# Kernel tuning notes

Hardware: AMD Instinct MI355X
Metric: run time of the kernel (lower is better)

Reference implementation:

```python
import jax, jax.numpy as jnp
import numpy as np

N = 500_000  # n_nodes == n_edges (required by the broadcast out * norm[:, None])
C_IN = 128
C_OUT = 128


def setup_inputs() -> dict:
    key = jax.random.key(0)
    k_x, k_e, k_w, k_b = jax.random.split(key, 4)
    x = jax.random.normal(k_x, (N, C_IN), dtype=jnp.float32)
    edge_index = jax.random.randint(k_e, (2, N), 0, N, dtype=jnp.int64)
    # Linear(in_channels, out_channels): weight [out, in], bias [out]
    bound = 1.0 / np.sqrt(C_IN)
    W = jax.random.uniform(k_w, (C_OUT, C_IN), minval=-bound, maxval=bound, dtype=jnp.float32)
    b = jax.random.uniform(k_b, (C_OUT,), minval=-bound, maxval=bound, dtype=jnp.float32)
    return {"x": x, "edge_index": edge_index, "W": W, "b": b}


def reference(x, edge_index, W, b):
    row, col = edge_index[0], edge_index[1]  # each [E], with E == N
    n = x.shape[0]
    out = x @ W.T + b  # [N, C_OUT]
    # degree via scatter-add of ones over row
    deg = jax.ops.segment_sum(jnp.ones(row.shape[0], dtype=x.dtype), row, num_segments=n)
    deg_inv_sqrt = jnp.where(deg > 0, jax.lax.rsqrt(jnp.where(deg > 0, deg, 1.0)), 0.0)
    norm = deg_inv_sqrt[row] * deg_inv_sqrt[col]  # [E] == [N]
    out = out * norm[:, None]  # broadcast relies on E == N (as in the torch source)
    # aggregated[row] += out[col]
    aggregated = jnp.zeros_like(out).at[row].add(out[col])
    return aggregated
```

## Files before the change

kernel.cpp:

```cpp
#include <hip/hip_runtime.h>

#define C 128

typedef __bf16 bf16_t;
typedef bf16_t bf16x8 __attribute__((ext_vector_type(8)));
typedef float f32x4 __attribute__((ext_vector_type(4)));

__global__ void deg_kernel(const int* __restrict__ row, int* __restrict__ deg, int e) {
    int i = blockIdx.x * blockDim.x + threadIdx.x;
    if (i < e) atomicAdd(&deg[row[i]], 1);
}

__global__ void wcvt_kernel(const float* __restrict__ W, bf16_t* __restrict__ Wb) {
    int i = blockIdx.x * blockDim.x + threadIdx.x;
    if (i < C * C) Wb[i] = (bf16_t)W[i];
}

__global__ __launch_bounds__(256) void scan1_kernel(const int* __restrict__ deg,
                                                    float* __restrict__ dis,
                                                    int* __restrict__ offs,
                                                    int* __restrict__ partials,
                                                    int* __restrict__ dhist, int n) {
    __shared__ int s[256];
    __shared__ int dh[32];
    const int tid = threadIdx.x;
    if (tid < 32) dh[tid] = 0;
    const int base = blockIdx.x * 1024 + tid * 4;
    int v[4];
    #pragma unroll
    for (int j = 0; j < 4; ++j) v[j] = (base + j < n) ? deg[base + j] : 0;
    #pragma unroll
    for (int j = 0; j < 4; ++j)
        if (base + j < n) dis[base + j] = v[j] > 0 ? rsqrtf((float)v[j]) : 0.f;
    int tsum = v[0] + v[1] + v[2] + v[3];
    s[tid] = tsum;
    __syncthreads();
    #pragma unroll
    for (int j = 0; j < 4; ++j)
        if (base + j < n) atomicAdd(&dh[min(v[j], 31)], 1);
    for (int off = 1; off < 256; off <<= 1) {
        int t = (tid >= off) ? s[tid - off] : 0;
        __syncthreads();
        s[tid] += t;
        __syncthreads();
    }
    int excl = s[tid] - tsum;
    #pragma unroll
    for (int j = 0; j < 4; ++j) {
        if (base + j < n) offs[base + j] = excl;
        excl += v[j];
    }
    if (tid == 255) partials[blockIdx.x] = s[255];
    if (tid < 32 && dh[tid] > 0) atomicAdd(&dhist[tid], dh[tid]);
}

__global__ __launch_bounds__(1024) void scan2_kernel(int* __restrict__ partials,
                                                     const int* __restrict__ dhist,
                                                     int* __restrict__ drun, int nb) {
    __shared__ int s[1024];
    const int tid = threadIdx.x;
    int v = (tid < nb) ? partials[tid] : 0;
    s[tid] = v;
    __syncthreads();
    for (int off = 1; off < 1024; off <<= 1) {
        int t = (tid >= off) ? s[tid - off] : 0;
        __syncthreads();
        s[tid] += t;
        __syncthreads();
    }
    if (tid < nb) partials[tid] = s[tid] - v;
    if (tid < 64) {
        int h = (tid < 32) ? dhist[tid] : 0;
        int c = h;
        #pragma unroll
        for (int off = 1; off < 32; off <<= 1) {
            int t = __shfl_up(c, off);
            if (tid >= off) c += t;
        }
        if (tid < 32) drun[tid] = c - h;
    }
}

__global__ __launch_bounds__(256) void permute_kernel(const int* __restrict__ deg,
                                                      int* __restrict__ drun,
                                                      int* __restrict__ perm, int n) {
    __shared__ int lh[32], lb[32];
    const int tid = threadIdx.x;
    const int i = blockIdx.x * 256 + tid;
    if (tid < 32) lh[tid] = 0;
    __syncthreads();
    int bin = 0, lr = 0;
    const bool valid = i < n;
    if (valid) {
        int d = deg[i];
        bin = min(d, 31);
        lr = atomicAdd(&lh[bin], 1);
    }
    __syncthreads();
    if (tid < 32 && lh[tid] > 0) lb[tid] = atomicAdd(&drun[tid], lh[tid]);
    __syncthreads();
    if (valid) perm[lb[bin] + lr] = i;
}

__global__ void bucket_kernel(const int* __restrict__ row, const int* __restrict__ col,
                              const int* __restrict__ offs, const int* __restrict__ partials,
                              const float* __restrict__ dis, int* __restrict__ cursor,
                              int2* __restrict__ csr_cw, int e) {
    int i = blockIdx.x * blockDim.x + threadIdx.x;
    if (i < e) {
        int r = row[i];
        int c = col[i];
        float w = dis[row[c]] * dis[col[c]];
        int pos = atomicAdd(&cursor[r], 1);
        int idx = offs[r] + partials[r >> 10] + pos;
        csr_cw[idx] = make_int2(c, __float_as_int(w));
    }
}

__global__ __launch_bounds__(256, 4) void fused_kernel(
        const f32x4* __restrict__ x4, const int2* __restrict__ csr_cw,
        const int* __restrict__ offs, const int* __restrict__ partials,
        const int* __restrict__ deg, const int* __restrict__ perm,
        const bf16x8* __restrict__ Wb8, const float* __restrict__ bias,
        float* __restrict__ out, int n)
{
    const int lane = threadIdx.x & 63;
    const int wave = threadIdx.x >> 6;
    const int m    = lane & 15;
    const int quad = lane >> 4;
    const long r0  = ((long)blockIdx.x * 4 + wave) * 16;
    if (r0 >= n) return;
    const int  pi = (int)r0 + m;
    const bool rv = pi < n;
    const int  prow  = rv ? perm[pi] : 0;
    const int  d     = rv ? deg[prow] : 0;
    const int  start = rv ? offs[prow] + partials[prow >> 10] : 0;

    f32x4 acc[8];
    #pragma unroll
    for (int i = 0; i < 8; ++i) acc[i] = (f32x4){0.f, 0.f, 0.f, 0.f};
    float sw = 0.f;

    int k = 0;
    for (; k + 2 <= d; k += 2) {
        const int2 cw0 = csr_cw[start + k];
        const int2 cw1 = csr_cw[start + k + 1];
        const float w0 = __int_as_float(cw0.y);
        const float w1 = __int_as_float(cw1.y);
        sw += w0 + w1;
        const f32x4* xr0 = x4 + (long)cw0.x * 32 + quad * 2;
        const f32x4* xr1 = x4 + (long)cw1.x * 32 + quad * 2;
        #pragma unroll
        for (int kc = 0; kc < 4; ++kc) {
            f32x4 u0 = xr0[kc * 8];
            f32x4 u1 = xr0[kc * 8 + 1];
            f32x4 v0 = xr1[kc * 8];
            f32x4 v1 = xr1[kc * 8 + 1];
            acc[kc * 2]     += w0 * u0;
            acc[kc * 2 + 1] += w0 * u1;
            acc[kc * 2]     += w1 * v0;
            acc[kc * 2 + 1] += w1 * v1;
        }
    }
    if (k < d) {
        const int2 cw = csr_cw[start + k];
        const float w = __int_as_float(cw.y);
        sw += w;
        const f32x4* xr = x4 + (long)cw.x * 32 + quad * 2;
        #pragma unroll
        for (int kc = 0; kc < 4; ++kc) {
            f32x4 u0 = xr[kc * 8];
            f32x4 u1 = xr[kc * 8 + 1];
            acc[kc * 2]     += w * u0;
            acc[kc * 2 + 1] += w * u1;
        }
    }

    bf16x8 a[4];
    #pragma unroll
    for (int kc = 0; kc < 4; ++kc) {
        #pragma unroll
        for (int j = 0; j < 4; ++j) {
            a[kc][j]     = (bf16_t)acc[kc * 2][j];
            a[kc][j + 4] = (bf16_t)acc[kc * 2 + 1][j];
        }
    }

    float cv[4];
    int   orow[4];
    #pragma unroll
    for (int v = 0; v < 4; ++v) {
        cv[v]   = __shfl(sw, quad * 4 + v);
        orow[v] = __shfl(prow, quad * 4 + v);
    }

    for (int t = 0; t < 8; ++t) {
        const int o = t * 16 + m;
        bf16x8 bf[4];
        #pragma unroll
        for (int kc = 0; kc < 4; ++kc)
            bf[kc] = Wb8[(long)o * 16 + kc * 4 + quad];
        f32x4 cacc = {0.f, 0.f, 0.f, 0.f};
        #pragma unroll
        for (int kc = 0; kc < 4; ++kc)
            cacc = __builtin_amdgcn_mfma_f32_16x16x32_bf16(a[kc], bf[kc], cacc, 0, 0, 0);
        const float bb = bias[o];
        #pragma unroll
        for (int v = 0; v < 4; ++v) {
            if (r0 + quad * 4 + v < n)
                __builtin_nontemporal_store(cacc[v] + cv[v] * bb,
                                            &out[(long)orow[v] * C + o]);
        }
    }
}

extern "C" void kernel_launch(void* const* d_in, const int* in_sizes, int n_in,
                              void* d_out, int out_size, void* d_ws, size_t ws_size,
                              hipStream_t stream) {
    const float* x  = (const float*)d_in[0];
    const int*   ei = (const int*)d_in[1];
    const float* W  = (const float*)d_in[2];
    const float* b  = (const float*)d_in[3];
    float* out = (float*)d_out;

    const int n = in_sizes[0] / C;
    const int e = in_sizes[1] / 2;
    const int* row = ei;
    const int* col = ei + e;

    int*   deg_i    = (int*)d_ws;
    int*   cursor   = deg_i + n;
    int*   offs     = cursor + n;
    int2*  csr_cw   = (int2*)(offs + n);
    float* dis      = (float*)(csr_cw + e);
    int*   perm     = (int*)(dis + n);
    int*   partials = perm + n;
    int*   dhist    = (int*)csr_cw;
    int*   drun     = dhist + 32;
    bf16_t* Wb      = (bf16_t*)cursor;

    const int nb = (n + 1023) / 1024;

    hipMemsetAsync(deg_i, 0, (size_t)2 * n * sizeof(int), stream);
    hipMemsetAsync(dhist, 0, 64 * sizeof(int), stream);

    deg_kernel<<<(e + 255) / 256, 256, 0, stream>>>(row, deg_i, e);
    scan1_kernel<<<nb, 256, 0, stream>>>(deg_i, dis, offs, partials, dhist, n);
    scan2_kernel<<<1, 1024, 0, stream>>>(partials, dhist, drun, nb);
    permute_kernel<<<(n + 255) / 256, 256, 0, stream>>>(deg_i, drun, perm, n);
    bucket_kernel<<<(e + 255) / 256, 256, 0, stream>>>(row, col, offs, partials, dis,
                                                       cursor, csr_cw, e);
    wcvt_kernel<<<(C * C + 255) / 256, 256, 0, stream>>>(W, Wb);

    int blocks = (n + 63) / 64;
    fused_kernel<<<blocks, 256, 0, stream>>>(
        (const f32x4*)x, csr_cw, offs, partials, deg_i, perm,
        (const bf16x8*)Wb, b, out, n);
}
```

Baseline: 622.2 us.

## Pack permuted row metadata and fast-path zero-degree row groups

The permutation now stores row id, degree and CSR start packed in one int2 per sorted slot. The fused kernel therefore does one coalesced load instead of dependent gathers from perm, deg, offs and partials. The degree sort is reversed so high-degree rows come first and zero-degree rows cluster at the end. Waves whose 16 rows all have zero degree then just write zeros and skip the MFMA work. Permute moves after bucket so perm2 can reuse the dis buffer, and the 20-bit row and 12-bit degree packing limits n and degree.

```diff
diff --git a/kernel.cpp b/kernel.cpp
--- a/kernel.cpp
+++ b/kernel.cpp
@@ -37,7 +37,7 @@
     __syncthreads();
     #pragma unroll
     for (int j = 0; j < 4; ++j)
-        if (base + j < n) atomicAdd(&dh[min(v[j], 31)], 1);
+        if (base + j < n) atomicAdd(&dh[31 - min(v[j], 31)], 1);
     for (int off = 1; off < 256; off <<= 1) {
         int t = (tid >= off) ? s[tid - off] : 0;
         __syncthreads();
@@ -79,27 +79,6 @@
         }
         if (tid < 32) drun[tid] = c - h;
     }
-}
-
-__global__ __launch_bounds__(256) void permute_kernel(const int* __restrict__ deg,
-                                                      int* __restrict__ drun,
-                                                      int* __restrict__ perm, int n) {
-    __shared__ int lh[32], lb[32];
-    const int tid = threadIdx.x;
-    const int i = blockIdx.x * 256 + tid;
-    if (tid < 32) lh[tid] = 0;
-    __syncthreads();
-    int bin = 0, lr = 0;
-    const bool valid = i < n;
-    if (valid) {
-        int d = deg[i];
-        bin = min(d, 31);
-        lr = atomicAdd(&lh[bin], 1);
-    }
-    __syncthreads();
-    if (tid < 32 && lh[tid] > 0) lb[tid] = atomicAdd(&drun[tid], lh[tid]);
-    __syncthreads();
-    if (valid) perm[lb[bin] + lr] = i;
 }
 
 __global__ void bucket_kernel(const int* __restrict__ row, const int* __restrict__ col,
@@ -117,12 +96,34 @@
     }
 }
 
+__global__ __launch_bounds__(256) void permute_kernel(const int* __restrict__ deg,
+                                                      const int* __restrict__ offs,
+                                                      const int* __restrict__ partials,
+                                                      int* __restrict__ drun,
+                                                      int2* __restrict__ perm2, int n) {
+    __shared__ int lh[32], lb[32];
+    const int tid = threadIdx.x;
+    const int i = blockIdx.x * 256 + tid;
+    if (tid < 32) lh[tid] = 0;
+    __syncthreads();
+    int bin = 0, lr = 0, d = 0;
+    const bool valid = i < n;
+    if (valid) {
+        d = deg[i];
+        bin = 31 - min(d, 31);
+        lr = atomicAdd(&lh[bin], 1);
+    }
+    __syncthreads();
+    if (tid < 32 && lh[tid] > 0) lb[tid] = atomicAdd(&drun[tid], lh[tid]);
+    __syncthreads();
+    if (valid)
+        perm2[lb[bin] + lr] = make_int2(i | (d << 20), offs[i] + partials[i >> 10]);
+}
+
 __global__ __launch_bounds__(256, 4) void fused_kernel(
         const f32x4* __restrict__ x4, const int2* __restrict__ csr_cw,
-        const int* __restrict__ offs, const int* __restrict__ partials,
-        const int* __restrict__ deg, const int* __restrict__ perm,
-        const bf16x8* __restrict__ Wb8, const float* __restrict__ bias,
-        float* __restrict__ out, int n)
+        const int2* __restrict__ perm2, const bf16x8* __restrict__ Wb8,
+        const float* __restrict__ bias, float* __restrict__ out, int n)
 {
     const int lane = threadIdx.x & 63;
     const int wave = threadIdx.x >> 6;
@@ -130,11 +131,29 @@
     const int quad = lane >> 4;
     const long r0  = ((long)blockIdx.x * 4 + wave) * 16;
     if (r0 >= n) return;
-    const int  pi = (int)r0 + m;
-    const bool rv = pi < n;
-    const int  prow  = rv ? perm[pi] : 0;
-    const int  d     = rv ? deg[prow] : 0;
-    const int  start = rv ? offs[prow] + partials[prow >> 10] : 0;
+    const int pi = (int)r0 + m;
+    int prow = 0, d = 0, start = 0;
+    if (pi < n) {
+        const int2 pk = perm2[pi];
+        prow  = pk.x & 0xFFFFF;
+        d     = ((unsigned)pk.x) >> 20;
+        start = pk.y;
+    }
+    int orow[4];
+    #pragma unroll
+    for (int v = 0; v < 4; ++v) orow[v] = __shfl(prow, quad * 4 + v);
+
+    if (__all(d == 0)) {
+        #pragma unroll
+        for (int t = 0; t < 8; ++t) {
+            const int o = t * 16 + m;
+            #pragma unroll
+            for (int v = 0; v < 4; ++v)
+                if (r0 + quad * 4 + v < n)
+                    __builtin_nontemporal_store(0.f, &out[(long)orow[v] * C + o]);
+        }
+        return;
+    }
 
     f32x4 acc[8];
     #pragma unroll
@@ -187,12 +206,8 @@
     }
 
     float cv[4];
-    int   orow[4];
-    #pragma unroll
-    for (int v = 0; v < 4; ++v) {
-        cv[v]   = __shfl(sw, quad * 4 + v);
-        orow[v] = __shfl(prow, quad * 4 + v);
-    }
+    #pragma unroll
+    for (int v = 0; v < 4; ++v) cv[v] = __shfl(sw, quad * 4 + v);
 
     for (int t = 0; t < 8; ++t) {
         const int o = t * 16 + m;
@@ -233,27 +248,28 @@
     int*   offs     = cursor + n;
     int2*  csr_cw   = (int2*)(offs + n);
     float* dis      = (float*)(csr_cw + e);
-    int*   perm     = (int*)(dis + n);
-    int*   partials = perm + n;
-    int*   dhist    = (int*)csr_cw;
-    int*   drun     = dhist + 32;
+    int*   perm_old = (int*)(dis + n);
+    int*   partials = perm_old + n;
+    int*   dhist    = partials + 512;
+    int*   drun     = partials + 576;
+    int2*  perm2    = (int2*)dis;
     bf16_t* Wb      = (bf16_t*)cursor;
 
     const int nb = (n + 1023) / 1024;
 
     hipMemsetAsync(deg_i, 0, (size_t)2 * n * sizeof(int), stream);
-    hipMemsetAsync(dhist, 0, 64 * sizeof(int), stream);
+    hipMemsetAsync(dhist, 0, 32 * sizeof(int), stream);
 
     deg_kernel<<<(e + 255) / 256, 256, 0, stream>>>(row, deg_i, e);
     scan1_kernel<<<nb, 256, 0, stream>>>(deg_i, dis, offs, partials, dhist, n);
     scan2_kernel<<<1, 1024, 0, stream>>>(partials, dhist, drun, nb);
-    permute_kernel<<<(n + 255) / 256, 256, 0, stream>>>(deg_i, drun, perm, n);
     bucket_kernel<<<(e + 255) / 256, 256, 0, stream>>>(row, col, offs, partials, dis,
                                                        cursor, csr_cw, e);
+    permute_kernel<<<(n + 255) / 256, 256, 0, stream>>>(deg_i, offs, partials, drun,
+                                                        perm2, n);
     wcvt_kernel<<<(C * C + 255) / 256, 256, 0, stream>>>(W, Wb);
 
     int blocks = (n + 63) / 64;
     fused_kernel<<<blocks, 256, 0, stream>>>(
-        (const f32x4*)x, csr_cw, offs, partials, deg_i, perm,
-        (const bf16x8*)Wb, b, out, n);
-}
+        (const f32x4*)x, csr_cw, perm2, (const bf16x8*)Wb, b, out, n);
+}
```

Measured after the change: 588.0 us. 1.06x faster.
